# Optimization experiments

Hardware: AMD Instinct MI355X
Metric: run time of the kernel (lower is better)

Reference implementation:

```python
import jax, jax.numpy as jnp
import numpy as np
from jax import lax

B, T, I, H = 128, 512, 2, 128   # batch, seq_len, input_size, hidden_size
H2 = H // 2                      # per-direction LSTM hidden


def _lstm_dir(x, Wih, Whh, bih, bhh):
    """Unidirectional LSTM over x:[B,T,in]. PyTorch gate order i,f,g,o.
    Returns (outputs [B,T,Hc], final_h [B,Hc])."""
    Hc = Whh.shape[1]
    b = bih + bhh

    def step(carry, xt):
        h, c = carry
        g = xt @ Wih.T + h @ Whh.T + b
        i, f, gg, o = jnp.split(g, 4, axis=-1)
        c = jax.nn.sigmoid(f) * c + jax.nn.sigmoid(i) * jnp.tanh(gg)
        h = jax.nn.sigmoid(o) * jnp.tanh(c)
        return (h, c), h

    h0 = jnp.zeros((x.shape[0], Hc), x.dtype)
    (hT, _), hs = lax.scan(step, (h0, h0), x.transpose(1, 0, 2))
    return hs.transpose(1, 0, 2), hT


def _bi_lstm(x, pf, pb):
    out_f, h_f = _lstm_dir(x, *pf)
    out_b, h_b = _lstm_dir(x[:, ::-1, :], *pb)
    out = jnp.concatenate([out_f, out_b[:, ::-1, :]], axis=-1)  # [B,T,H]
    hidden = jnp.concatenate([h_f, h_b], axis=-1)               # [B,H]
    return out, hidden


def _f_hid_mve(hidden_l, hidden_list, Wih, Whh, bih, bhh):
    """Custom LSTMCell scan; input = cat(hidden_list[:,t,:], hidden_l) (2H dims),
    cell size H. Collects the CELL state C each step (as in the source)."""
    Hc = Whh.shape[1]
    b = bih + bhh

    def step(carry, xt):
        h, c = carry
        g = jnp.concatenate([xt, hidden_l], axis=-1) @ Wih.T + h @ Whh.T + b
        i, f, gg, o = jnp.split(g, 4, axis=-1)
        c = jax.nn.sigmoid(f) * c + jax.nn.sigmoid(i) * jnp.tanh(gg)
        h = jax.nn.sigmoid(o) * jnp.tanh(c)
        return (h, c), c

    h0 = jnp.zeros((hidden_list.shape[0], Hc), hidden_list.dtype)
    _, cs = lax.scan(step, (h0, h0), hidden_list.transpose(1, 0, 2))
    return cs.transpose(1, 0, 2)  # [B,T,H]


def _f_hid_sim(hi, Wi, bi, Wc, bc, Wo, bo):
    C = jax.nn.sigmoid(hi @ Wi.T + bi) * jnp.tanh(hi @ Wc.T + bc)
    return jax.nn.sigmoid(hi @ Wo.T + bo) * jnp.tanh(C) + hi


def setup_inputs() -> dict:
    key = jax.random.key(0)
    ks = jax.random.split(key, 32)
    n = lambda k, s: jax.random.normal(k, s, dtype=jnp.float32) * 0.1
    inp = {}
    names = ["anchor_nearest_input", "anchor_farest_input", "nearest_input",
             "farest_input", "trajectory_anchor_input",
             "trajectory_nearest_input", "trajectory_farest_input"]
    for j, nm in enumerate(names):
        inp[nm] = jax.random.normal(ks[j], (B, T, I), dtype=jnp.float32)
    # shared bidirectional LSTM params (per-direction hidden H2)
    inp["Wih_f"] = n(ks[7], (4 * H2, I)); inp["Whh_f"] = n(ks[8], (4 * H2, H2))
    inp["bih_f"] = n(ks[9], (4 * H2,));  inp["bhh_f"] = n(ks[10], (4 * H2,))
    inp["Wih_b"] = n(ks[11], (4 * H2, I)); inp["Whh_b"] = n(ks[12], (4 * H2, H2))
    inp["bih_b"] = n(ks[13], (4 * H2,));  inp["bhh_b"] = n(ks[14], (4 * H2,))
    # f_hid_mve LSTMCell(2H -> H)
    inp["mve_Wih"] = n(ks[15], (4 * H, 2 * H)); inp["mve_Whh"] = n(ks[16], (4 * H, H))
    inp["mve_bih"] = n(ks[17], (4 * H,));       inp["mve_bhh"] = n(ks[18], (4 * H,))
    # f_hid_sim linears (H -> H)
    inp["sim_Wi"] = n(ks[19], (H, H)); inp["sim_bi"] = jnp.zeros((H,), jnp.float32)
    inp["sim_Wc"] = n(ks[20], (H, H)); inp["sim_bc"] = jnp.zeros((H,), jnp.float32)
    inp["sim_Wo"] = n(ks[21], (H, H)); inp["sim_bo"] = jnp.zeros((H,), jnp.float32)
    return inp


def reference(anchor_nearest_input, anchor_farest_input, nearest_input,
              farest_input, trajectory_anchor_input, trajectory_nearest_input,
              trajectory_farest_input,
              Wih_f, Whh_f, bih_f, bhh_f, Wih_b, Whh_b, bih_b, bhh_b,
              mve_Wih, mve_Whh, mve_bih, mve_bhh,
              sim_Wi, sim_bi, sim_Wc, sim_bc, sim_Wo, sim_bo):
    pf = (Wih_f, Whh_f, bih_f, bhh_f)
    pb = (Wih_b, Whh_b, bih_b, bhh_b)

    _, an_hidden = _bi_lstm(anchor_nearest_input, pf, pb)
    _, af_hidden = _bi_lstm(anchor_farest_input, pf, pb)
    _, n_hidden = _bi_lstm(nearest_input, pf, pb)
    _, f_hidden = _bi_lstm(farest_input, pf, pb)
    ta_out, ta_hidden = _bi_lstm(trajectory_anchor_input, pf, pb)
    tn_out, tn_hidden = _bi_lstm(trajectory_nearest_input, pf, pb)
    tf_out, tf_hidden = _bi_lstm(trajectory_farest_input, pf, pb)

    m_anchor = _f_hid_mve(ta_hidden, ta_out, mve_Wih, mve_Whh, mve_bih, mve_bhh)
    m_nearest = _f_hid_mve(tn_hidden, tn_out, mve_Wih, mve_Whh, mve_bih, mve_bhh)
    m_farest = _f_hid_mve(tf_hidden, tf_out, mve_Wih, mve_Whh, mve_bih, mve_bhh)

    sim = lambda h: _f_hid_sim(h, sim_Wi, sim_bi, sim_Wc, sim_bc, sim_Wo, sim_bo)
    an_v, af_v = sim(an_hidden), sim(af_hidden)
    n_v, f_v = sim(n_hidden), sim(f_hidden)
    t_v, tn_v, tf_v = sim(ta_hidden), sim(tn_hidden), sim(tf_hidden)

    l2 = lambda a, b: jnp.exp(-jnp.linalg.norm(a - b, ord=2, axis=-1))
    return (l2(an_v, n_v), l2(af_v, f_v), l2(t_v, tn_v), l2(t_v, tf_v),
            m_anchor, m_nearest, m_farest)
```

## Files before the change

kernel.cpp:

```cpp
#include <hip/hip_runtime.h>
#include <hip/hip_bf16.h>

#define DEV __device__ __forceinline__

constexpr int BB  = 128;
constexpr int TT  = 512;
constexpr int HH  = 128;
constexpr int H2  = 64;
constexpr int GM  = 512;

constexpr float L2E = 1.4426950408889634f;
constexpr float K2  = 2.0f * L2E;

typedef __attribute__((ext_vector_type(8))) short bf16x8;
typedef __attribute__((ext_vector_type(4))) float f32x4;

#define MFMA16(a_, b_, c_) __builtin_amdgcn_mfma_f32_16x16x32_bf16((a_), (b_), (c_), 0, 0, 0)

#define BAR_LDS() asm volatile("s_waitcnt lgkmcnt(0)\n\ts_barrier" ::: "memory")

DEV float gscale(int q) { return (q == 2) ? K2 : -L2E; }

DEV float fexp2(float x) { return __builtin_amdgcn_exp2f(x); }
DEV float frcp(float x)  { return __builtin_amdgcn_rcpf(x); }
DEV float rcp1p(float e) { return frcp(1.f + e); }

DEV unsigned short f2bf(float x) {
    __hip_bfloat16 h = __float2bfloat16(x);
    unsigned short u;
    __builtin_memcpy(&u, &h, 2);
    return u;
}
DEV float asf(unsigned int u) {
    float f;
    __builtin_memcpy(&f, &u, 4);
    return f;
}
DEV unsigned int pk2(float lo, float hi) {
    __hip_bfloat162 b2 = __float22bfloat162_rn(make_float2(lo, hi));
    unsigned int u;
    __builtin_memcpy(&u, &b2, 4);
    return u;
}
DEV f32x4 unp4(unsigned int a, unsigned int b) {
    f32x4 v;
    v[0] = asf(a << 16); v[1] = asf(a & 0xffff0000u);
    v[2] = asf(b << 16); v[3] = asf(b & 0xffff0000u);
    return v;
}
DEV bf16x8 pack8(const float* f) {
    bf16x8 v;
#pragma unroll
    for (int e = 0; e < 8; ++e) v[e] = (short)f2bf(f[e]);
    return v;
}

DEV float cellup(const f32x4& acc, float& cst) {
    float Ai = fexp2(acc[0]);
    float Bg = fexp2(acc[2]);
    float sf = rcp1p(fexp2(acc[1]));
    float ig = (Bg - 1.f) * frcp((1.f + Ai) * (1.f + Bg));
    cst = __builtin_fmaf(sf, cst, ig);
    float Cc = fexp2(K2 * cst);
    float Do = fexp2(acc[3]);
    return (Cc - 1.f) * frcp((1.f + Do) * (1.f + Cc));
}

struct BiArgs {
    const float* x[7];
    const float* Wih[2];
    const float* Whh[2];
    const float* bih[2];
    const float* bhh[2];
    unsigned short* outs_bf;
    float* hid;
};

__global__ __launch_bounds__(512) void k_bilstm_mfma(BiArgs a) {
    const int blk  = blockIdx.x;
    const int prob = blk >> 3;
    const int b0   = (blk & 7) * 16;
    const int tid  = threadIdx.x;
    const int dir  = tid >> 8;
    const int w    = (tid >> 6) & 3;
    const int l    = tid & 63;
    const int lg   = l >> 4;
    const int lc   = l & 15;

    const float* Whh = a.Whh[dir];
    const float* Wih = a.Wih[dir];
    const float* bih = a.bih[dir];
    const float* bhh = a.bhh[dir];

    const float sw = gscale(lc & 3);
    bf16x8 wf[4][2];
#pragma unroll
    for (int mt = 0; mt < 4; ++mt) {
#pragma unroll
        for (int kh = 0; kh < 2; ++kh) {
            int orow = (lc & 3) * H2 + 16 * w + 4 * (lc >> 2) + mt;
            float tmp[8];
#pragma unroll
            for (int e = 0; e < 8; ++e)
                tmp[e] = Whh[(size_t)orow * H2 + 32 * kh + 8 * lg + e] * sw;
            wf[mt][kh] = pack8(tmp);
        }
    }
    float bia[4][4], wx0[4][4], wx1[4][4];
#pragma unroll
    for (int mt = 0; mt < 4; ++mt)
#pragma unroll
        for (int r = 0; r < 4; ++r) {
            int orow = r * H2 + 16 * w + 4 * lg + mt;
            float s = gscale(r);
            bia[mt][r] = (bih[orow] + bhh[orow]) * s;
            wx0[mt][r] = Wih[orow * 2 + 0] * s;
            wx1[mt][r] = Wih[orow * 2 + 1] * s;
        }

    __shared__ unsigned short Hb[2][2][8][16][8];
    ((unsigned long long*)&Hb[tid >> 8][0][0][0][0])[tid & 255] = 0ULL;

    const bool isTraj = (prob >= 4);
    unsigned short* outp = a.outs_bf + (size_t)(isTraj ? (prob - 4) : 0) * BB * TT * HH;
    const float2* xg2 = (const float2*)a.x[prob];
    const int c = b0 + lc;

    float cst[4] = {0.f, 0.f, 0.f, 0.f};
    int cur = 0;
    float2 xrA = xg2[(size_t)c * TT + (dir ? TT - 1 : 0)];
    float2 xrB = xg2[(size_t)c * TT + (dir ? TT - 2 : 1)];
    __syncthreads();

#define BI_BODY(XR, T_)                                                          \
    {                                                                            \
        const int t = (T_);                                                      \
        f32x4 acc[4];                                                            \
        _Pragma("unroll")                                                        \
        for (int mt = 0; mt < 4; ++mt) {                                         \
            f32x4 v;                                                             \
            _Pragma("unroll")                                                    \
            for (int r = 0; r < 4; ++r)                                          \
                v[r] = __builtin_fmaf(wx0[mt][r], XR.x,                          \
                        __builtin_fmaf(wx1[mt][r], XR.y, bia[mt][r]));           \
            acc[mt] = v;                                                         \
        }                                                                        \
        {                                                                        \
            int tn = (t + 2 < TT) ? t + 2 : t;                                   \
            XR = xg2[(size_t)c * TT + (dir ? TT - 1 - tn : tn)];                 \
        }                                                                        \
        _Pragma("unroll")                                                        \
        for (int kh = 0; kh < 2; ++kh) {                                         \
            bf16x8 bfrag = *(const bf16x8*)&Hb[dir][cur][4 * kh + lg][lc][0];    \
            _Pragma("unroll")                                                    \
            for (int mt = 0; mt < 4; ++mt)                                       \
                acc[mt] = MFMA16(wf[mt][kh], bfrag, acc[mt]);                    \
        }                                                                        \
        const int nxt = cur ^ 1;                                                 \
        const int tcol = dir ? (TT - 1 - t) : t;                                 \
        float4 h4;                                                               \
        float* hp4 = &h4.x;                                                      \
        _Pragma("unroll")                                                        \
        for (int mt = 0; mt < 4; ++mt)                                           \
            hp4[mt] = cellup(acc[mt], cst[mt]);                                  \
        uint2 hpk = make_uint2(pk2(h4.x, h4.y), pk2(h4.z, h4.w));                \
        {                                                                        \
            int pp = 16 * w + 4 * lg;                                            \
            *(uint2*)&Hb[dir][nxt][pp >> 3][lc][pp & 7] = hpk;                   \
        }                                                                        \
        if (isTraj)                                                              \
            *(uint2*)&outp[((size_t)c * TT + tcol) * HH + dir * H2               \
                           + 16 * w + 4 * lg] = hpk;                             \
        if (t == TT - 1)                                                         \
            *(float4*)&a.hid[((size_t)prob * BB + c) * HH + dir * H2             \
                             + 16 * w + 4 * lg] = h4;                            \
        BAR_LDS();                                                               \
        cur = nxt;                                                               \
    }

    for (int t2 = 0; t2 < TT; t2 += 2) {
        BI_BODY(xrA, t2)
        BI_BODY(xrB, t2 + 1)
    }
#undef BI_BODY
}

__global__ void k_wxB(const float* __restrict__ Wm, unsigned short* __restrict__ WxB) {
    int idx = blockIdx.x * 256 + threadIdx.x;
    int p = idx >> 7, k = idx & 127;
    int j = (p & 3) * HH + (p >> 2);
    WxB[idx] = f2bf(Wm[(size_t)j * (2 * HH) + k] * gscale(p & 3));
}

__global__ __launch_bounds__(256) void k_hp(const float* __restrict__ hidl,
                                            const float* __restrict__ Wih,
                                            const float* __restrict__ bih,
                                            const float* __restrict__ bhh,
                                            float* __restrict__ hp) {
    int traj = blockIdx.x, b = blockIdx.y;
    int j = threadIdx.x;
    __shared__ float hs[HH];
    if (j < HH) hs[j] = hidl[((size_t)traj * BB + b) * HH + j];
    __syncthreads();
    const float4* hs4 = (const float4*)hs;
#pragma unroll
    for (int rr = 0; rr < 2; ++rr) {
        int row = j + 256 * rr;
        float acc = bih[row] + bhh[row];
        const float4* w4 = (const float4*)(Wih + (size_t)row * (2 * HH) + HH);
#pragma unroll
        for (int k4 = 0; k4 < HH / 4; ++k4) {
            float4 wv = w4[k4], hv = hs4[k4];
            acc += wv.x * hv.x + wv.y * hv.y + wv.z * hv.z + wv.w * hv.w;
        }
        int p = 4 * (row & 127) + (row >> 7);
        hp[((size_t)traj * BB + b) * GM + p] = acc * gscale(row >> 7);
    }
}

__global__ __launch_bounds__(256) void k_xproj_mfma(
    const unsigned short* __restrict__ outs_bf,
    const unsigned short* __restrict__ WxB,
    const float* __restrict__ hp,
    unsigned short* __restrict__ xpb) {
    const int mb   = blockIdx.x;
    const int pb   = blockIdx.y;
    const int traj = blockIdx.z;
    const int tid  = threadIdx.x;
    const int w = tid >> 6, l = tid & 63, lg = l >> 4, lc = l & 15;
    const int m0 = mb * 128;
    const int p0 = pb * 128;
    const int c  = m0 >> 9;

    __shared__ unsigned short Xs[128 * 128];
    __shared__ unsigned short Ps[128 * 128];

    const uint4* xg4 = (const uint4*)(outs_bf + ((size_t)traj * (BB * TT) + m0) * HH);
    const uint4* pg4 = (const uint4*)(WxB + (size_t)p0 * HH);
#pragma unroll
    for (int i = 0; i < 8; ++i) {
        int j = i * 256 + tid;
        int byte = j * 16;
        int row = byte >> 8;
        int sb = byte ^ ((row & 7) << 4);
        *(uint4*)((char*)Xs + sb) = xg4[j];
        *(uint4*)((char*)Ps + sb) = pg4[j];
    }
    __syncthreads();

    bf16x8 xfrag[2][4];
#pragma unroll
    for (int xt = 0; xt < 2; ++xt)
#pragma unroll
        for (int kh = 0; kh < 4; ++kh) {
            int row = 32 * w + 16 * xt + lc;
            int byte = row * 256 + 64 * kh + 16 * lg;
            xfrag[xt][kh] = *(const bf16x8*)((const char*)Xs + (byte ^ ((row & 7) << 4)));
        }
    f32x4 acc[8][2];
#pragma unroll
    for (int pt = 0; pt < 8; ++pt)
#pragma unroll
        for (int xt = 0; xt < 2; ++xt)
#pragma unroll
            for (int r = 0; r < 4; ++r) acc[pt][xt][r] = 0.f;

#pragma unroll
    for (int pt = 0; pt < 8; ++pt) {
        bf16x8 pf[4];
#pragma unroll
        for (int kh = 0; kh < 4; ++kh) {
            int row = 16 * pt + lc;
            int byte = row * 256 + 64 * kh + 16 * lg;
            pf[kh] = *(const bf16x8*)((const char*)Ps + (byte ^ ((row & 7) << 4)));
        }
#pragma unroll
        for (int kh = 0; kh < 4; ++kh)
#pragma unroll
            for (int xt = 0; xt < 2; ++xt)
                acc[pt][xt] = MFMA16(pf[kh], xfrag[xt][kh], acc[pt][xt]);
    }
    __syncthreads();

#pragma unroll
    for (int pt = 0; pt < 8; ++pt) {
        float4 hv = *(const float4*)&hp[(((size_t)traj * BB + c)) * GM + p0 + 16 * pt + 4 * lg];
#pragma unroll
        for (int xt = 0; xt < 2; ++xt) {
            int mloc = 32 * w + 16 * xt + lc;
            int byte = mloc * 256 + (16 * pt + 4 * lg) * 2;
            uint2 u = make_uint2(pk2(acc[pt][xt][0] + hv.x, acc[pt][xt][1] + hv.y),
                                 pk2(acc[pt][xt][2] + hv.z, acc[pt][xt][3] + hv.w));
            *(uint2*)((char*)Ps + (byte ^ ((mloc & 7) << 4))) = u;
        }
    }
    __syncthreads();

    unsigned short* Cg = xpb + ((size_t)traj * (BB * TT) + m0) * GM + p0;
#pragma unroll
    for (int i = 0; i < 8; ++i) {
        int j = i * 256 + tid;
        int r = j >> 4;
        int cb = (j & 15) * 16;
        uint4 v = *(const uint4*)((const char*)Ps + ((r * 256 + cb) ^ ((r & 7) << 4)));
        *(uint4*)((char*)(Cg + (size_t)r * GM) + cb) = v;
    }
}

struct MveArgs {
    const unsigned short* xp;
    const float* Whh;
    float* mout;
};

__global__ __launch_bounds__(512) void k_mve_mfma(MveArgs a) {
    const int blk  = blockIdx.x;
    const int traj = blk >> 3;
    const int b0   = (blk & 7) * 16;
    const int tid  = threadIdx.x;
    const int w    = tid >> 6;
    const int l    = tid & 63;
    const int lg   = l >> 4;
    const int lc   = l & 15;
    const int c    = b0 + lc;

    const float sw = gscale(lc & 3);
    bf16x8 wf[4][4];
#pragma unroll
    for (int mt = 0; mt < 4; ++mt) {
#pragma unroll
        for (int kh = 0; kh < 4; ++kh) {
            int orow = (lc & 3) * HH + 16 * w + 4 * (lc >> 2) + mt;
            float tmp[8];
#pragma unroll
            for (int e = 0; e < 8; ++e)
                tmp[e] = a.Whh[(size_t)orow * HH + 32 * kh + 8 * lg + e] * sw;
            wf[mt][kh] = pack8(tmp);
        }
    }

    __shared__ unsigned short Hb[2][16][16][8];
    ((unsigned long long*)Hb)[tid] = 0ULL;

    const unsigned short* xrow = a.xp + (size_t)traj * BB * TT * GM
                               + (size_t)c * TT * GM + 64 * w + 16 * lg;
    float* mop = a.mout + (size_t)traj * BB * TT * HH
               + (size_t)c * TT * HH + 16 * w + 4 * lg;

    float cst[4] = {0.f, 0.f, 0.f, 0.f};
    int cur = 0;
    uint4 xqA0 = *(const uint4*)xrow;
    uint4 xqA1 = *(const uint4*)(xrow + 8);
    uint4 xqB0 = *(const uint4*)(xrow + GM);
    uint4 xqB1 = *(const uint4*)(xrow + GM + 8);
    __syncthreads();

#define MVE_BODY(XQ0, XQ1, T_)                                                   \
    {                                                                            \
        const int t = (T_);                                                      \
        f32x4 acc[4];                                                            \
        acc[0] = unp4(XQ0.x, XQ0.y);                                             \
        acc[1] = unp4(XQ0.z, XQ0.w);                                             \
        acc[2] = unp4(XQ1.x, XQ1.y);                                             \
        acc[3] = unp4(XQ1.z, XQ1.w);                                             \
        {                              \
            const unsigned short* pf = xrow                                      \
                + (size_t)((t + 2 < TT) ? t + 2 : t) * GM;                       \
            XQ0 = *(const uint4*)pf;                                             \
            XQ1 = *(const uint4*)(pf + 8);                                       \
        }                                                                        \
        _Pragma("unroll")                                                        \
        for (int kh = 0; kh < 4; ++kh) {                                         \
            bf16x8 bfrag = *(const bf16x8*)&Hb[cur][4 * kh + lg][lc][0];         \
            _Pragma("unroll")                                                    \
            for (int mt = 0; mt < 4; ++mt)                                       \
                acc[mt] = MFMA16(wf[mt][kh], bfrag, acc[mt]);                    \
        }                                                                        \
        const int nxt = cur ^ 1;                                                 \
        f32x4 cs4;                                                               \
        float h8[4];                                                             \
        _Pragma("unroll")                                                        \
        for (int mt = 0; mt < 4; ++mt) {                                         \
            h8[mt] = cellup(acc[mt], cst[mt]);                                   \
            cs4[mt] = cst[mt];                                                   \
        }                                                                        \
        {                                                                        \
            int pp = 16 * w + 4 * lg;                                            \
            *(uint2*)&Hb[nxt][pp >> 3][lc][pp & 7] =                             \
                make_uint2(pk2(h8[0], h8[1]), pk2(h8[2], h8[3]));                \
        }                                                                        \
                \
        __builtin_nontemporal_store(cs4, (f32x4*)(mop + (size_t)t * HH));        \
        BAR_LDS();                                                               \
        cur = nxt;                                                               \
    }

    for (int t2 = 0; t2 < TT; t2 += 2) {
        MVE_BODY(xqA0, xqA1, t2)
        MVE_BODY(xqB0, xqB1, t2 + 1)
    }
#undef MVE_BODY
}

__global__ __launch_bounds__(128) void k_sim(const float* __restrict__ hid,
                                             const float* __restrict__ Wi, const float* __restrict__ bi,
                                             const float* __restrict__ Wc, const float* __restrict__ bc,
                                             const float* __restrict__ Wo, const float* __restrict__ bo,
                                             float* __restrict__ simv) {
    int which = blockIdx.x >> 7;
    int b = blockIdx.x & 127;
    int j = threadIdx.x;
    __shared__ float hs[HH];
    hs[j] = hid[((size_t)which * BB + b) * HH + j];
    __syncthreads();
    float ai = bi[j], ac = bc[j], ao = bo[j];
    const float4* wi4 = (const float4*)(Wi + (size_t)j * HH);
    const float4* wc4 = (const float4*)(Wc + (size_t)j * HH);
    const float4* wo4 = (const float4*)(Wo + (size_t)j * HH);
#pragma unroll
    for (int k4 = 0; k4 < HH / 4; ++k4) {
        float4 h = ((const float4*)hs)[k4];
        float4 vi = wi4[k4]; ai += vi.x*h.x + vi.y*h.y + vi.z*h.z + vi.w*h.w;
        float4 vc = wc4[k4]; ac += vc.x*h.x + vc.y*h.y + vc.z*h.z + vc.w*h.w;
        float4 vo = wo4[k4]; ao += vo.x*h.x + vo.y*h.y + vo.z*h.z + vo.w*h.w;
    }
    float Cv = (1.f / (1.f + __expf(-ai))) * tanhf(ac);
    float v = (1.f / (1.f + __expf(-ao))) * tanhf(Cv) + hs[j];
    simv[((size_t)which * BB + b) * HH + j] = v;
}

__global__ __launch_bounds__(64) void k_l2(const float* __restrict__ simv,
                                           float* __restrict__ out) {
    int p = blockIdx.x >> 7;
    int b = blockIdx.x & 127;
    int aw, cw;
    switch (p) {
        case 0: aw = 0; cw = 2; break;
        case 1: aw = 1; cw = 3; break;
        case 2: aw = 4; cw = 5; break;
        default: aw = 4; cw = 6; break;
    }
    int l = threadIdx.x;
    const float* va = simv + ((size_t)aw * BB + b) * HH;
    const float* vc = simv + ((size_t)cw * BB + b) * HH;
    float d0 = va[l] - vc[l];
    float d1 = va[l + 64] - vc[l + 64];
    float s = d0 * d0 + d1 * d1;
#pragma unroll
    for (int m = 32; m >= 1; m >>= 1) s += __shfl_xor(s, m, 64);
    if (l == 0) out[p * BB + b] = expf(-sqrtf(s));
}

extern "C" void kernel_launch(void* const* d_in, const int* in_sizes, int n_in,
                              void* d_out_v, int out_size, void* d_ws, size_t ws_size,
                              hipStream_t stream) {
    const float* mWih  = (const float*)d_in[15];
    const float* mWhh  = (const float*)d_in[16];
    const float* mbih  = (const float*)d_in[17];
    const float* mbhh  = (const float*)d_in[18];
    const float* sWi   = (const float*)d_in[19];
    const float* sbi   = (const float*)d_in[20];
    const float* sWc   = (const float*)d_in[21];
    const float* sbc   = (const float*)d_in[22];
    const float* sWo   = (const float*)d_in[23];
    const float* sbo   = (const float*)d_in[24];

    constexpr size_t OUTSBF_LEN = (size_t)3 * BB * TT * HH;
    constexpr size_t HID_LEN    = (size_t)7 * BB * HH;
    constexpr size_t WXB_LEN    = (size_t)GM * HH;
    constexpr size_t SIMV_LEN   = HID_LEN;
    constexpr size_t HP_LEN     = (size_t)3 * BB * GM;
    constexpr size_t XP_LEN     = (size_t)3 * BB * TT * GM;

    char* ws = (char*)d_ws;
    unsigned short* outs_bf = (unsigned short*)ws;                 ws += OUTSBF_LEN * 2;
    float*          hid     = (float*)ws;                          ws += HID_LEN * 4;
    unsigned short* WxB     = (unsigned short*)ws;                 ws += WXB_LEN * 2;
    float*          simv    = (float*)ws;                          ws += SIMV_LEN * 4;
    float*          hp      = (float*)ws;                          ws += HP_LEN * 4;
    unsigned short* xpb     = (unsigned short*)ws;                 ws += XP_LEN * 2;

    float* dout = (float*)d_out_v;
    float* mout = dout + 512;

    BiArgs ba;
    for (int i = 0; i < 7; ++i) ba.x[i] = (const float*)d_in[i];
    ba.Wih[0] = (const float*)d_in[7];  ba.Whh[0] = (const float*)d_in[8];
    ba.bih[0] = (const float*)d_in[9];  ba.bhh[0] = (const float*)d_in[10];
    ba.Wih[1] = (const float*)d_in[11]; ba.Whh[1] = (const float*)d_in[12];
    ba.bih[1] = (const float*)d_in[13]; ba.bhh[1] = (const float*)d_in[14];
    ba.outs_bf = outs_bf; ba.hid = hid;

    k_wxB<<<256, 256, 0, stream>>>(mWih, WxB);
    k_bilstm_mfma<<<56, 512, 0, stream>>>(ba);
    k_hp<<<dim3(3, BB), 256, 0, stream>>>(hid + (size_t)4 * BB * HH, mWih, mbih, mbhh, hp);

    dim3 gx(BB * TT / 128, GM / 128, 3);
    k_xproj_mfma<<<gx, 256, 0, stream>>>(outs_bf, WxB, hp, xpb);

    MveArgs ma;
    ma.xp = xpb; ma.Whh = mWhh; ma.mout = mout;
    k_mve_mfma<<<24, 512, 0, stream>>>(ma);

    k_sim<<<7 * BB, 128, 0, stream>>>(hid, sWi, sbi, sWc, sbc, sWo, sbo, simv);
    k_l2<<<4 * BB, 64, 0, stream>>>(simv, dout);
}
```

Measured before the change: 906.4 us.

## Double waves per block in recurrent LSTM kernels to halve per-wave serial work

Both recurrent kernels (bi-LSTM and MVE) now launch 1024 threads per block instead of 512. Each wave owns half as many gate rows (2 MFMA tiles instead of 4), which shortens the per-timestep dependent MFMA and cell-update chain on each wave. In exchange, hidden-state writes to LDS and global memory become scalar 16-bit or 32-bit stores rather than packed vectors. More waves also take part in the per-step barrier, which may raise synchronisation cost.

```diff
diff --git a/kernel.cpp b/kernel.cpp
--- a/kernel.cpp
+++ b/kernel.cpp
@@ -76,13 +76,13 @@
     float* hid;
 };
 
-__global__ __launch_bounds__(512) void k_bilstm_mfma(BiArgs a) {
+__global__ __launch_bounds__(1024) void k_bilstm_mfma(BiArgs a) {
     const int blk  = blockIdx.x;
     const int prob = blk >> 3;
     const int b0   = (blk & 7) * 16;
     const int tid  = threadIdx.x;
-    const int dir  = tid >> 8;
-    const int w    = (tid >> 6) & 3;
+    const int dir  = tid >> 9;
+    const int w    = (tid >> 6) & 7;
     const int l    = tid & 63;
     const int lg   = l >> 4;
     const int lc   = l & 15;
@@ -93,12 +93,12 @@
     const float* bhh = a.bhh[dir];
 
     const float sw = gscale(lc & 3);
-    bf16x8 wf[4][2];
-#pragma unroll
-    for (int mt = 0; mt < 4; ++mt) {
+    bf16x8 wf[2][2];
+#pragma unroll
+    for (int mt = 0; mt < 2; ++mt) {
 #pragma unroll
         for (int kh = 0; kh < 2; ++kh) {
-            int orow = (lc & 3) * H2 + 16 * w + 4 * (lc >> 2) + mt;
+            int orow = (lc & 3) * H2 + 8 * w + (lc >> 2) + 4 * mt;
             float tmp[8];
 #pragma unroll
             for (int e = 0; e < 8; ++e)
@@ -106,12 +106,12 @@
             wf[mt][kh] = pack8(tmp);
         }
     }
-    float bia[4][4], wx0[4][4], wx1[4][4];
-#pragma unroll
-    for (int mt = 0; mt < 4; ++mt)
+    float bia[2][4], wx0[2][4], wx1[2][4];
+#pragma unroll
+    for (int mt = 0; mt < 2; ++mt)
 #pragma unroll
         for (int r = 0; r < 4; ++r) {
-            int orow = r * H2 + 16 * w + 4 * lg + mt;
+            int orow = r * H2 + 8 * w + lg + 4 * mt;
             float s = gscale(r);
             bia[mt][r] = (bih[orow] + bhh[orow]) * s;
             wx0[mt][r] = Wih[orow * 2 + 0] * s;
@@ -119,14 +119,15 @@
         }
 
     __shared__ unsigned short Hb[2][2][8][16][8];
-    ((unsigned long long*)&Hb[tid >> 8][0][0][0][0])[tid & 255] = 0ULL;
+    if ((tid & 511) < 256)
+        ((unsigned long long*)&Hb[tid >> 9][0][0][0][0])[tid & 255] = 0ULL;
 
     const bool isTraj = (prob >= 4);
     unsigned short* outp = a.outs_bf + (size_t)(isTraj ? (prob - 4) : 0) * BB * TT * HH;
     const float2* xg2 = (const float2*)a.x[prob];
     const int c = b0 + lc;
 
-    float cst[4] = {0.f, 0.f, 0.f, 0.f};
+    float cst[2] = {0.f, 0.f};
     int cur = 0;
     float2 xrA = xg2[(size_t)c * TT + (dir ? TT - 1 : 0)];
     float2 xrB = xg2[(size_t)c * TT + (dir ? TT - 2 : 1)];
@@ -135,9 +136,9 @@
 #define BI_BODY(XR, T_)                                                          \
     {                                                                            \
         const int t = (T_);                                                      \
-        f32x4 acc[4];                                                            \
+        f32x4 acc[2];                                                            \
         _Pragma("unroll")                                                        \
-        for (int mt = 0; mt < 4; ++mt) {                                         \
+        for (int mt = 0; mt < 2; ++mt) {                                         \
             f32x4 v;                                                             \
             _Pragma("unroll")                                                    \
             for (int r = 0; r < 4; ++r)                                          \
@@ -153,27 +154,28 @@
         for (int kh = 0; kh < 2; ++kh) {                                         \
             bf16x8 bfrag = *(const bf16x8*)&Hb[dir][cur][4 * kh + lg][lc][0];    \
             _Pragma("unroll")                                                    \
-            for (int mt = 0; mt < 4; ++mt)                                       \
+            for (int mt = 0; mt < 2; ++mt)                                       \
                 acc[mt] = MFMA16(wf[mt][kh], bfrag, acc[mt]);                    \
         }                                                                        \
         const int nxt = cur ^ 1;                                                 \
         const int tcol = dir ? (TT - 1 - t) : t;                                 \
-        float4 h4;                                                               \
-        float* hp4 = &h4.x;                                                      \
-        _Pragma("unroll")                                                        \
-        for (int mt = 0; mt < 4; ++mt)                                           \
-            hp4[mt] = cellup(acc[mt], cst[mt]);                                  \
-        uint2 hpk = make_uint2(pk2(h4.x, h4.y), pk2(h4.z, h4.w));                \
-        {                                                                        \
-            int pp = 16 * w + 4 * lg;                                            \
-            *(uint2*)&Hb[dir][nxt][pp >> 3][lc][pp & 7] = hpk;                   \
-        }                                                                        \
-        if (isTraj)                                                              \
-            *(uint2*)&outp[((size_t)c * TT + tcol) * HH + dir * H2               \
-                           + 16 * w + 4 * lg] = hpk;                             \
-        if (t == TT - 1)                                                         \
-            *(float4*)&a.hid[((size_t)prob * BB + c) * HH + dir * H2             \
-                             + 16 * w + 4 * lg] = h4;                            \
+        float h0 = cellup(acc[0], cst[0]);                                       \
+        float h1 = cellup(acc[1], cst[1]);                                       \
+        unsigned short hb0 = f2bf(h0), hb1 = f2bf(h1);                           \
+        Hb[dir][nxt][w][lc][lg]     = hb0;                                       \
+        Hb[dir][nxt][w][lc][lg + 4] = hb1;                                       \
+        if (isTraj) {                                                            \
+            unsigned short* op = &outp[((size_t)c * TT + tcol) * HH              \
+                                       + dir * H2 + 8 * w + lg];                 \
+            op[0] = hb0;                                                         \
+            op[4] = hb1;                                                         \
+        }                                                                        \
+        if (t == TT - 1) {                                                       \
+            float* hd = &a.hid[((size_t)prob * BB + c) * HH + dir * H2           \
+                               + 8 * w + lg];                                    \
+            hd[0] = h0;                                                          \
+            hd[4] = h1;                                                          \
+        }                                                                        \
         BAR_LDS();                                                               \
         cur = nxt;                                                               \
     }
@@ -313,7 +315,7 @@
     float* mout;
 };
 
-__global__ __launch_bounds__(512) void k_mve_mfma(MveArgs a) {
+__global__ __launch_bounds__(1024) void k_mve_mfma(MveArgs a) {
     const int blk  = blockIdx.x;
     const int traj = blk >> 3;
     const int b0   = (blk & 7) * 16;
@@ -325,12 +327,12 @@
     const int c    = b0 + lc;
 
     const float sw = gscale(lc & 3);
-    bf16x8 wf[4][4];
-#pragma unroll
-    for (int mt = 0; mt < 4; ++mt) {
+    bf16x8 wf[2][4];
+#pragma unroll
+    for (int mt = 0; mt < 2; ++mt) {
 #pragma unroll
         for (int kh = 0; kh < 4; ++kh) {
-            int orow = (lc & 3) * HH + 16 * w + 4 * (lc >> 2) + mt;
+            int orow = (lc & 3) * HH + 8 * w + (lc >> 2) + 4 * mt;
             float tmp[8];
 #pragma unroll
             for (int e = 0; e < 8; ++e)
@@ -340,57 +342,50 @@
     }
 
     __shared__ unsigned short Hb[2][16][16][8];
-    ((unsigned long long*)Hb)[tid] = 0ULL;
+    if (tid < 512) ((unsigned long long*)Hb)[tid] = 0ULL;
 
     const unsigned short* xrow = a.xp + (size_t)traj * BB * TT * GM
-                               + (size_t)c * TT * GM + 64 * w + 16 * lg;
+                               + (size_t)c * TT * GM + 32 * w + 4 * lg;
     float* mop = a.mout + (size_t)traj * BB * TT * HH
-               + (size_t)c * TT * HH + 16 * w + 4 * lg;
-
-    float cst[4] = {0.f, 0.f, 0.f, 0.f};
+               + (size_t)c * TT * HH + 8 * w + lg;
+
+    float cst[2] = {0.f, 0.f};
     int cur = 0;
-    uint4 xqA0 = *(const uint4*)xrow;
-    uint4 xqA1 = *(const uint4*)(xrow + 8);
-    uint4 xqB0 = *(const uint4*)(xrow + GM);
-    uint4 xqB1 = *(const uint4*)(xrow + GM + 8);
+    uint2 xqA0 = *(const uint2*)xrow;
+    uint2 xqA1 = *(const uint2*)(xrow + 16);
+    uint2 xqB0 = *(const uint2*)(xrow + GM);
+    uint2 xqB1 = *(const uint2*)(xrow + GM + 16);
     __syncthreads();
 
 #define MVE_BODY(XQ0, XQ1, T_)                                                   \
     {                                                                            \
         const int t = (T_);                                                      \
-        f32x4 acc[4];                                                            \
+        f32x4 acc[2];                                                            \
         acc[0] = unp4(XQ0.x, XQ0.y);                                             \
-        acc[1] = unp4(XQ0.z, XQ0.w);                                             \
-        acc[2] = unp4(XQ1.x, XQ1.y);                                             \
-        acc[3] = unp4(XQ1.z, XQ1.w);                                             \
+        acc[1] = unp4(XQ1.x, XQ1.y);                                             \
         {                              \
             const unsigned short* pf = xrow                                      \
                 + (size_t)((t + 2 < TT) ? t + 2 : t) * GM;                       \
-            XQ0 = *(const uint4*)pf;                                             \
-            XQ1 = *(const uint4*)(pf + 8);                                       \
+            XQ0 = *(const uint2*)pf;                                             \
+            XQ1 = *(const uint2*)(pf + 16);                                      \
         }                                                                        \
         _Pragma("unroll")                                                        \
         for (int kh = 0; kh < 4; ++kh) {                                         \
             bf16x8 bfrag = *(const bf16x8*)&Hb[cur][4 * kh + lg][lc][0];         \
             _Pragma("unroll")                                                    \
-            for (int mt = 0; mt < 4; ++mt)                                       \
+            for (int mt = 0; mt < 2; ++mt)                                       \
                 acc[mt] = MFMA16(wf[mt][kh], bfrag, acc[mt]);                    \
         }                                                                        \
         const int nxt = cur ^ 1;                                                 \
-        f32x4 cs4;                                                               \
-        float h8[4];                                                             \
-        _Pragma("unroll")                                                        \
-        for (int mt = 0; mt < 4; ++mt) {                                         \
-            h8[mt] = cellup(acc[mt], cst[mt]);                                   \
-            cs4[mt] = cst[mt];                                                   \
-        }                                                                        \
-        {                                                                        \
-            int pp = 16 * w + 4 * lg;                                            \
-            *(uint2*)&Hb[nxt][pp >> 3][lc][pp & 7] =                             \
-                make_uint2(pk2(h8[0], h8[1]), pk2(h8[2], h8[3]));                \
-        }                                                                        \
-                \
-        __builtin_nontemporal_store(cs4, (f32x4*)(mop + (size_t)t * HH));        \
+        float h0 = cellup(acc[0], cst[0]);                                       \
+        float h1 = cellup(acc[1], cst[1]);                                       \
+        Hb[nxt][w][lc][lg]     = f2bf(h0);                                       \
+        Hb[nxt][w][lc][lg + 4] = f2bf(h1);                                       \
+        {         \
+            float* mo = mop + (size_t)t * HH;                                    \
+            __builtin_nontemporal_store(cst[0], mo);                             \
+            __builtin_nontemporal_store(cst[1], mo + 4);                         \
+        }                                                                        \
         BAR_LDS();                                                               \
         cur = nxt;                                                               \
     }
@@ -492,7 +487,7 @@
     ba.outs_bf = outs_bf; ba.hid = hid;
 
     k_wxB<<<256, 256, 0, stream>>>(mWih, WxB);
-    k_bilstm_mfma<<<56, 512, 0, stream>>>(ba);
+    k_bilstm_mfma<<<56, 1024, 0, stream>>>(ba);
     k_hp<<<dim3(3, BB), 256, 0, stream>>>(hid + (size_t)4 * BB * HH, mWih, mbih, mbhh, hp);
 
     dim3 gx(BB * TT / 128, GM / 128, 3);
@@ -500,7 +495,7 @@
 
     MveArgs ma;
     ma.xp = xpb; ma.Whh = mWhh; ma.mout = mout;
-    k_mve_mfma<<<24, 512, 0, stream>>>(ma);
+    k_mve_mfma<<<24, 1024, 0, stream>>>(ma);
 
     k_sim<<<7 * BB, 128, 0, stream>>>(hid, sWi, sbi, sWc, sbc, sWo, sbo, simv);
     k_l2<<<4 * BB, 64, 0, stream>>>(simv, dout);
```

Result: slower. 1.477 ms (+62.9%).

## Split MVE recurrence across 16 waves per block to halve per-wave MFMA chain

Applied to the files above, without the earlier changes.

The sequential MVE LSTM kernel now launches 1024 threads per block instead of 512, so each wave owns two output tiles instead of four. This halves each wave's MFMA work, weight registers and cell updates per timestep, shortening the serial critical path of the recurrence. In exchange, more waves meet at every per-step barrier, and the per-lane loads and stores become smaller (8-byte float2 stores instead of 16-byte nontemporal ones).

```diff
diff --git a/kernel.cpp b/kernel.cpp
--- a/kernel.cpp
+++ b/kernel.cpp
@@ -313,7 +313,7 @@
     float* mout;
 };
 
-__global__ __launch_bounds__(512) void k_mve_mfma(MveArgs a) {
+__global__ __launch_bounds__(1024) void k_mve_mfma(MveArgs a) {
     const int blk  = blockIdx.x;
     const int traj = blk >> 3;
     const int b0   = (blk & 7) * 16;
@@ -325,12 +325,12 @@
     const int c    = b0 + lc;
 
     const float sw = gscale(lc & 3);
-    bf16x8 wf[4][4];
-#pragma unroll
-    for (int mt = 0; mt < 4; ++mt) {
+    bf16x8 wf[2][4];
+#pragma unroll
+    for (int mt = 0; mt < 2; ++mt) {
 #pragma unroll
         for (int kh = 0; kh < 4; ++kh) {
-            int orow = (lc & 3) * HH + 16 * w + 4 * (lc >> 2) + mt;
+            int orow = (lc & 3) * HH + 8 * w + 2 * (lc >> 2) + mt;
             float tmp[8];
 #pragma unroll
             for (int e = 0; e < 8; ++e)
@@ -340,64 +340,51 @@
     }
 
     __shared__ unsigned short Hb[2][16][16][8];
-    ((unsigned long long*)Hb)[tid] = 0ULL;
+    if (tid < 512) ((unsigned long long*)Hb)[tid] = 0ULL;
 
     const unsigned short* xrow = a.xp + (size_t)traj * BB * TT * GM
-                               + (size_t)c * TT * GM + 64 * w + 16 * lg;
+                               + (size_t)c * TT * GM + 32 * w + 8 * lg;
     float* mop = a.mout + (size_t)traj * BB * TT * HH
-               + (size_t)c * TT * HH + 16 * w + 4 * lg;
-
-    float cst[4] = {0.f, 0.f, 0.f, 0.f};
+               + (size_t)c * TT * HH + 8 * w + 2 * lg;
+
+    float cst[2] = {0.f, 0.f};
     int cur = 0;
-    uint4 xqA0 = *(const uint4*)xrow;
-    uint4 xqA1 = *(const uint4*)(xrow + 8);
-    uint4 xqB0 = *(const uint4*)(xrow + GM);
-    uint4 xqB1 = *(const uint4*)(xrow + GM + 8);
-    __syncthreads();
-
-#define MVE_BODY(XQ0, XQ1, T_)                                                   \
+    uint4 xqA = *(const uint4*)xrow;
+    uint4 xqB = *(const uint4*)(xrow + GM);
+    __syncthreads();
+
+#define MVE_BODY(XQ, T_)                                                         \
     {                                                                            \
         const int t = (T_);                                                      \
-        f32x4 acc[4];                                                            \
-        acc[0] = unp4(XQ0.x, XQ0.y);                                             \
-        acc[1] = unp4(XQ0.z, XQ0.w);                                             \
-        acc[2] = unp4(XQ1.x, XQ1.y);                                             \
-        acc[3] = unp4(XQ1.z, XQ1.w);                                             \
-        {                              \
+        f32x4 acc[2];                                                            \
+        acc[0] = unp4(XQ.x, XQ.y);                                               \
+        acc[1] = unp4(XQ.z, XQ.w);                                               \
+        {                               \
             const unsigned short* pf = xrow                                      \
                 + (size_t)((t + 2 < TT) ? t + 2 : t) * GM;                       \
-            XQ0 = *(const uint4*)pf;                                             \
-            XQ1 = *(const uint4*)(pf + 8);                                       \
+            XQ = *(const uint4*)pf;                                              \
         }                                                                        \
         _Pragma("unroll")                                                        \
         for (int kh = 0; kh < 4; ++kh) {                                         \
             bf16x8 bfrag = *(const bf16x8*)&Hb[cur][4 * kh + lg][lc][0];         \
             _Pragma("unroll")                                                    \
-            for (int mt = 0; mt < 4; ++mt)                                       \
+            for (int mt = 0; mt < 2; ++mt)                                       \
                 acc[mt] = MFMA16(wf[mt][kh], bfrag, acc[mt]);                    \
         }                                                                        \
         const int nxt = cur ^ 1;                                                 \
-        f32x4 cs4;                                                               \
-        float h8[4];                                                             \
-        _Pragma("unroll")                                                        \
-        for (int mt = 0; mt < 4; ++mt) {                                         \
-            h8[mt] = cellup(acc[mt], cst[mt]);                                   \
-            cs4[mt] = cst[mt];                                                   \
-        }                                                                        \
-        {                                                                        \
-            int pp = 16 * w + 4 * lg;                                            \
-            *(uint2*)&Hb[nxt][pp >> 3][lc][pp & 7] =                             \
-                make_uint2(pk2(h8[0], h8[1]), pk2(h8[2], h8[3]));                \
-        }                                                                        \
-                \
-        __builtin_nontemporal_store(cs4, (f32x4*)(mop + (size_t)t * HH));        \
+        float h0 = cellup(acc[0], cst[0]);                                       \
+        float h1 = cellup(acc[1], cst[1]);                                       \
+        *(unsigned int*)&Hb[nxt][w][lc][2 * lg] = pk2(h0, h1);                   \
+        {                        \
+            *(float2*)(mop + (size_t)t * HH) = make_float2(cst[0], cst[1]);      \
+        }                                                                        \
         BAR_LDS();                                                               \
         cur = nxt;                                                               \
     }
 
     for (int t2 = 0; t2 < TT; t2 += 2) {
-        MVE_BODY(xqA0, xqA1, t2)
-        MVE_BODY(xqB0, xqB1, t2 + 1)
+        MVE_BODY(xqA, t2)
+        MVE_BODY(xqB, t2 + 1)
     }
 #undef MVE_BODY
 }
@@ -500,7 +487,7 @@
 
     MveArgs ma;
     ma.xp = xpb; ma.Whh = mWhh; ma.mout = mout;
-    k_mve_mfma<<<24, 512, 0, stream>>>(ma);
+    k_mve_mfma<<<24, 1024, 0, stream>>>(ma);
 
     k_sim<<<7 * BB, 128, 0, stream>>>(hid, sWi, sbi, sWc, sbc, sWo, sbo, simv);
     k_l2<<<4 * BB, 64, 0, stream>>>(simv, dout);
```

Result: slower. 963.5 us (+6.3%).
